# Performance work log

Measured on AMD Instinct MI355X. Metric: run time of the kernel, lower is better.

Reference implementation:

```python
import jax, jax.numpy as jnp
import numpy as np

B, C, N = 16, 512, 2048
MAXH, MAXW = 70, 40   # max_height, max_width with f_size=1
GY, GX = 80, 48       # virtual coordinate grid for input generation
BIG = 1_000_000


def setup_inputs() -> dict:
    key = jax.random.key(0)
    kf, kp, kv = jax.random.split(key, 3)
    features = jax.random.normal(kf, (B, C, N), dtype=jnp.float32)
    cells = jax.vmap(lambda k: jax.random.permutation(k, GY * GX)[:N])(
        jax.random.split(kp, B))
    ys = (cells // GX).astype(jnp.int32)
    xs = (cells % GX).astype(jnp.int32)
    valid = jax.random.bernoulli(kv, 0.9, (B, N)).at[:, 0].set(True)
    ys = jnp.where(valid, ys, -1)
    xs = jnp.where(valid, xs, -1)
    backend_feature = jnp.zeros((C, 1, 1), dtype=jnp.float32)  # dummy='zero'
    return {"features": features, "backend_feature": backend_feature,
            "ys": ys, "xs": xs}


def _one_sample(f, y, x, backend):
    # f: [C, N], y/x: [N] int, backend: [C, 1, 1]
    valid = y > -1
    min_y = jnp.min(jnp.where(valid, y, BIG))
    max_y = jnp.max(jnp.where(valid, y, -BIG))
    min_x = jnp.min(jnp.where(valid, x, BIG))
    max_x = jnp.max(jnp.where(valid, x, -BIG))
    h = max_y - min_y + 1
    w = max_x - min_x + 1
    # transpose if width > height
    trans = w > h
    yy = jnp.where(trans, x - min_x, y - min_y)
    xx = jnp.where(trans, y - min_y, x - min_x)
    H2 = jnp.where(trans, w, h)
    W2 = jnp.where(trans, h, w)
    # validation-mode centered crop/pad -> a single shift per axis
    hd = H2 - MAXH
    wd = W2 - MAXW
    sy = jnp.where(hd > 0, -((hd + 1) // 2), (1 - hd) // 2)
    sx = jnp.where(wd > 0, -((wd + 1) // 2), (1 - wd) // 2)
    oy = jnp.where(valid, yy + sy, -BIG)  # force drop for invalid points
    ox = jnp.where(valid, xx + sx, -BIG)
    canvas = jnp.zeros((C, MAXH, MAXW), f.dtype).at[:, oy, ox].set(f, mode='drop')
    mask = jnp.zeros((MAXH, MAXW), bool).at[oy, ox].set(True, mode='drop')
    # blend: real pixels from canvas, dummy backend elsewhere
    return jnp.where(mask[None], canvas, backend)


def reference(features, backend_feature, ys, xs):
    return jax.vmap(_one_sample, in_axes=(0, 0, 0, None))(
        features, ys, xs, backend_feature)
```

## Files before the change

kernel.cpp:

```cpp
#include <hip/hip_runtime.h>

#define BB 16
#define CC 512
#define NN 2048
#define MAXH 70
#define MAXW 40
#define NPIX (MAXH * MAXW)
#define BIGC 1000000

__global__ __launch_bounds__(256) void fused_map_kernel(
    const float* __restrict__ feat, const float* __restrict__ backend,
    const int* __restrict__ ys, const int* __restrict__ xs,
    float* __restrict__ out)
{
    const int plane = blockIdx.x;
    const int b = plane >> 9;
    const int c = plane & (CC - 1);
    const int tid = threadIdx.x;
    const int* __restrict__ y = ys + b * NN;
    const int* __restrict__ x = xs + b * NN;

    __shared__ int smap[NPIX];
    __shared__ int s0[256], s1[256], s2[256], s3[256];

    for (int p = tid; p < NPIX; p += 256) smap[p] = -1;

    int mny = BIGC, mxy = -BIGC, mnx = BIGC, mxx = -BIGC;
    for (int n = tid; n < NN; n += 256) {
        int yy = y[n];
        if (yy > -1) {
            int xx = x[n];
            mny = min(mny, yy); mxy = max(mxy, yy);
            mnx = min(mnx, xx); mxx = max(mxx, xx);
        }
    }
    s0[tid] = mny; s1[tid] = mxy; s2[tid] = mnx; s3[tid] = mxx;
    __syncthreads();
    for (int s = 128; s > 0; s >>= 1) {
        if (tid < s) {
            s0[tid] = min(s0[tid], s0[tid + s]);
            s1[tid] = max(s1[tid], s1[tid + s]);
            s2[tid] = min(s2[tid], s2[tid + s]);
            s3[tid] = max(s3[tid], s3[tid + s]);
        }
        __syncthreads();
    }
    const int min_y = s0[0], max_y = s1[0], min_x = s2[0], max_x = s3[0];
    const int h = max_y - min_y + 1;
    const int w = max_x - min_x + 1;
    const int trans = (w > h) ? 1 : 0;
    const int H2 = trans ? w : h;
    const int W2 = trans ? h : w;
    const int hd = H2 - MAXH;
    const int wd = W2 - MAXW;
    const int sy = (hd > 0) ? -((hd + 1) / 2) : ((1 - hd) / 2);
    const int sx = (wd > 0) ? -((wd + 1) / 2) : ((1 - wd) / 2);

    for (int n = tid; n < NN; n += 256) {
        int yy0 = y[n];
        if (yy0 <= -1) continue;
        int ry = yy0 - min_y;
        int rx = x[n] - min_x;
        int oy = (trans ? rx : ry) + sy;
        int ox = (trans ? ry : rx) + sx;
        if (oy < 0) oy += MAXH;
        if (ox < 0) ox += MAXW;
        if (oy >= 0 && oy < MAXH && ox >= 0 && ox < MAXW)
            atomicMax(&smap[oy * MAXW + ox], n);
    }
    __syncthreads();

    const float bv = backend[c];
    const float* __restrict__ frow = feat + (size_t)plane * NN;
    float4* __restrict__ orow4 = (float4*)(out + (size_t)plane * NPIX);

    for (int p4 = tid; p4 < NPIX / 4; p4 += 256) {
        const int base = p4 * 4;
        int a0 = smap[base + 0];
        int a1 = smap[base + 1];
        int a2 = smap[base + 2];
        int a3 = smap[base + 3];
        float4 v;
        v.x = (a0 >= 0) ? frow[a0] : bv;
        v.y = (a1 >= 0) ? frow[a1] : bv;
        v.z = (a2 >= 0) ? frow[a2] : bv;
        v.w = (a3 >= 0) ? frow[a3] : bv;
        orow4[p4] = v;
    }
}

extern "C" void kernel_launch(void* const* d_in, const int* in_sizes, int n_in,
                              void* d_out, int out_size, void* d_ws, size_t ws_size,
                              hipStream_t stream) {
    const float* feat    = (const float*)d_in[0];
    const float* backend = (const float*)d_in[1];
    const int*   ys      = (const int*)d_in[2];
    const int*   xs      = (const int*)d_in[3];
    float* out = (float*)d_out;

    fused_map_kernel<<<BB * CC, 256, 0, stream>>>(feat, backend, ys, xs, out);
}
```

Measured before the change: 188.8 us.

## Split map building into per-sample kernel and reuse map across channels

The pixel-to-point index map depended only on the sample but was rebuilt by every one of the 8192 channel blocks, costing a reduction, atomics and coordinate loads each time. It is now built once per sample by a 16-block kernel and written to workspace. A second kernel reads the map with vector loads and gathers features, using nontemporal stores for the output. This adds a second launch and a dependency on workspace size, and falls back to the fused kernel when the workspace is too small.

Result: no change. 185.1 us (-2.0%).

```diff
diff --git a/kernel.cpp b/kernel.cpp
--- a/kernel.cpp
+++ b/kernel.cpp
@@ -7,6 +7,95 @@
 #define MAXW 40
 #define NPIX (MAXH * MAXW)
 #define BIGC 1000000
+
+typedef float  f32x4 __attribute__((ext_vector_type(4)));
+typedef int    i32x4 __attribute__((ext_vector_type(4)));
+
+__global__ __launch_bounds__(256) void build_map_kernel(
+    const int* __restrict__ ys, const int* __restrict__ xs,
+    int* __restrict__ srcmap)
+{
+    const int b = blockIdx.x;
+    const int tid = threadIdx.x;
+    const int* __restrict__ y = ys + b * NN;
+    const int* __restrict__ x = xs + b * NN;
+
+    __shared__ int smap[NPIX];
+    __shared__ int s0[256], s1[256], s2[256], s3[256];
+
+    for (int p = tid; p < NPIX; p += 256) smap[p] = -1;
+
+    int mny = BIGC, mxy = -BIGC, mnx = BIGC, mxx = -BIGC;
+    for (int n = tid; n < NN; n += 256) {
+        int yy = y[n];
+        if (yy > -1) {
+            int xx = x[n];
+            mny = min(mny, yy); mxy = max(mxy, yy);
+            mnx = min(mnx, xx); mxx = max(mxx, xx);
+        }
+    }
+    s0[tid] = mny; s1[tid] = mxy; s2[tid] = mnx; s3[tid] = mxx;
+    __syncthreads();
+    for (int s = 128; s > 0; s >>= 1) {
+        if (tid < s) {
+            s0[tid] = min(s0[tid], s0[tid + s]);
+            s1[tid] = max(s1[tid], s1[tid + s]);
+            s2[tid] = min(s2[tid], s2[tid + s]);
+            s3[tid] = max(s3[tid], s3[tid + s]);
+        }
+        __syncthreads();
+    }
+    const int min_y = s0[0], max_y = s1[0], min_x = s2[0], max_x = s3[0];
+    const int h = max_y - min_y + 1;
+    const int w = max_x - min_x + 1;
+    const int trans = (w > h) ? 1 : 0;
+    const int H2 = trans ? w : h;
+    const int W2 = trans ? h : w;
+    const int hd = H2 - MAXH;
+    const int wd = W2 - MAXW;
+    const int sy = (hd > 0) ? -((hd + 1) / 2) : ((1 - hd) / 2);
+    const int sx = (wd > 0) ? -((wd + 1) / 2) : ((1 - wd) / 2);
+
+    for (int n = tid; n < NN; n += 256) {
+        int yy0 = y[n];
+        if (yy0 <= -1) continue;
+        int ry = yy0 - min_y;
+        int rx = x[n] - min_x;
+        int oy = (trans ? rx : ry) + sy;
+        int ox = (trans ? ry : rx) + sx;
+        if (oy < 0) oy += MAXH;
+        if (ox < 0) ox += MAXW;
+        if (oy >= 0 && oy < MAXH && ox >= 0 && ox < MAXW)
+            atomicMax(&smap[oy * MAXW + ox], n);
+    }
+    __syncthreads();
+
+    int* __restrict__ g = srcmap + b * NPIX;
+    for (int p = tid; p < NPIX; p += 256) g[p] = smap[p];
+}
+
+__global__ __launch_bounds__(256) void fill_out_kernel(
+    const float* __restrict__ feat, const float* __restrict__ backend,
+    const int* __restrict__ srcmap, float* __restrict__ out)
+{
+    const int plane = blockIdx.x;
+    const int b = plane >> 9;
+    const int c = plane & (CC - 1);
+    const float bv = backend[c];
+    const float* __restrict__ frow = feat + (size_t)plane * NN;
+    const i32x4* __restrict__ smap4 = (const i32x4*)(srcmap + b * NPIX);
+    f32x4* __restrict__ orow4 = (f32x4*)(out + (size_t)plane * NPIX);
+
+    for (int p4 = threadIdx.x; p4 < NPIX / 4; p4 += 256) {
+        i32x4 s = smap4[p4];
+        f32x4 v;
+        v.x = (s.x >= 0) ? frow[s.x] : bv;
+        v.y = (s.y >= 0) ? frow[s.y] : bv;
+        v.z = (s.z >= 0) ? frow[s.z] : bv;
+        v.w = (s.w >= 0) ? frow[s.w] : bv;
+        __builtin_nontemporal_store(v, &orow4[p4]);
+    }
+}
 
 __global__ __launch_bounds__(256) void fused_map_kernel(
     const float* __restrict__ feat, const float* __restrict__ backend,
@@ -72,7 +161,7 @@
 
     const float bv = backend[c];
     const float* __restrict__ frow = feat + (size_t)plane * NN;
-    float4* __restrict__ orow4 = (float4*)(out + (size_t)plane * NPIX);
+    f32x4* __restrict__ orow4 = (f32x4*)(out + (size_t)plane * NPIX);
 
     for (int p4 = tid; p4 < NPIX / 4; p4 += 256) {
         const int base = p4 * 4;
@@ -80,7 +169,7 @@
         int a1 = smap[base + 1];
         int a2 = smap[base + 2];
         int a3 = smap[base + 3];
-        float4 v;
+        f32x4 v;
         v.x = (a0 >= 0) ? frow[a0] : bv;
         v.y = (a1 >= 0) ? frow[a1] : bv;
         v.z = (a2 >= 0) ? frow[a2] : bv;
@@ -98,5 +187,12 @@
     const int*   xs      = (const int*)d_in[3];
     float* out = (float*)d_out;
 
-    fused_map_kernel<<<BB * CC, 256, 0, stream>>>(feat, backend, ys, xs, out);
+    const size_t need = (size_t)BB * NPIX * sizeof(int);
+    if (ws_size >= need) {
+        int* srcmap = (int*)d_ws;
+        build_map_kernel<<<BB, 256, 0, stream>>>(ys, xs, srcmap);
+        fill_out_kernel<<<BB * CC, 256, 0, stream>>>(feat, backend, srcmap, out);
+    } else {
+        fused_map_kernel<<<BB * CC, 256, 0, stream>>>(feat, backend, ys, xs, out);
+    }
 }
```
